# Kernel optimization log

Measured on AMD Instinct MI355X. Metric: run time of the kernel, lower is better.

Reference implementation:

```python
import jax, jax.numpy as jnp
import numpy as np

NUM_NODE = 64   # number of FPS nodes
NSAMPLE = 64    # ball-query / knn group size
RADIUS = 0.3    # first ball-query radius
K_INTERP = 3    # knn for upsample interpolation
BN_EPS = 1e-5


def sqdist(a, b):
    # a [B,S,3], b [B,N,3] -> squared distances [B,S,N]
    return (jnp.sum(a * a, -1)[:, :, None] + jnp.sum(b * b, -1)[:, None, :]
            - 2.0 * jnp.einsum('bsc,bnc->bsn', a, b))


def index_points(points, idx):
    # points [B,C,N] or [B,C,N,1]; idx [B,...] -> gathered [B,C,...]
    if points.ndim == 4:
        points = points[..., 0]
    return jax.vmap(lambda p, i: p[:, i])(points, idx)


def farthest_point_sample(xyz, npoint):
    # xyz [B,3,N] -> idx [B,npoint]; deterministic start at index 0
    B, C, N = xyz.shape

    def body(carry, _):
        dist, far = carry
        centroid = jnp.take_along_axis(xyz, far[:, None, None], axis=2)  # [B,3,1]
        d = jnp.sum((xyz - centroid) ** 2, axis=1)                       # [B,N]
        dist = jnp.minimum(dist, d)
        nxt = jnp.argmax(dist, axis=-1)
        return (dist, nxt), far

    init = (jnp.full((B, N), 1e10, xyz.dtype), jnp.zeros((B,), jnp.int32))
    _, idxs = jax.lax.scan(body, init, None, length=npoint)
    return idxs.T  # [B,npoint]


def query_ball_point(radius, nsample, xyz, new_xyz):
    # xyz [B,3,N], new_xyz [B,3,S] -> group idx [B,S,nsample]
    N = xyz.shape[2]
    sqr = sqdist(jnp.transpose(new_xyz, (0, 2, 1)), jnp.transpose(xyz, (0, 2, 1)))  # [B,S,N]
    if radius is not None:
        idx = jnp.broadcast_to(jnp.arange(N, dtype=jnp.int32), sqr.shape)
        idx = jnp.where(sqr > radius * radius, N, idx)
        idx = jnp.sort(idx, axis=-1)[:, :, :nsample]
        first = idx[:, :, :1]
        idx = jnp.where(idx == N, first, idx)  # pad misses with first hit
    else:
        idx = jnp.argsort(sqr, axis=-1)[:, :, :nsample].astype(jnp.int32)  # knn
    return idx


def _forward(input_fea, input_loc, pred_w, res_w, res_b, bn_gamma, bn_beta):
    # input_fea [B,C,N,1], input_loc [B,3,N]
    fidx = farthest_point_sample(input_loc, NUM_NODE)        # [B,S]
    fpoint_loc = index_points(input_loc, fidx)               # [B,3,S]
    fpoint_fea = index_points(input_fea, fidx)               # [B,C,S]

    gidx = query_ball_point(RADIUS, NSAMPLE, input_loc, fpoint_loc)  # [B,S,K]
    group_fea = index_points(input_fea, gidx) - fpoint_fea[..., None]  # [B,C,S,K]

    # pred_offset: 1x1 conv (no bias) + tanh
    seman = jnp.tanh(jnp.einsum('oc,bcsk->bosk', pred_w, group_fea))  # [B,3,S,K]

    group_loc = index_points(input_loc, gidx) - fpoint_loc[..., None]  # [B,3,S,K]
    node_offset = jnp.mean(seman * group_loc, axis=-1)       # [B,3,S]
    node_loc = fpoint_loc + node_offset                      # [B,3,S]

    gidx2 = query_ball_point(None, NSAMPLE, input_loc, node_loc)  # knn, [B,S,K]

    # residual branch: 1x1 conv + BatchNorm (training-mode batch stats) + ReLU
    res = jnp.einsum('oc,bcnk->bonk', res_w, input_fea) + res_b[None, :, None, None]
    mean = jnp.mean(res, axis=(0, 2, 3), keepdims=True)
    var = jnp.var(res, axis=(0, 2, 3), keepdims=True)
    res = (res - mean) * jax.lax.rsqrt(var + BN_EPS)
    res = jax.nn.relu(res * bn_gamma[None, :, None, None] + bn_beta[None, :, None, None])

    group_res = index_points(res, gidx2)                     # [B,F,S,K]
    node_fea = jnp.max(group_res, axis=-1, keepdims=True)    # [B,F,S,1]

    # upsample_inter: inverse-distance weighted 3-NN interpolation back to N points
    d = sqdist(jnp.transpose(input_loc, (0, 2, 1)), jnp.transpose(node_loc, (0, 2, 1)))  # [B,N,S]
    neg_d, kidx = jax.lax.top_k(-d, K_INTERP)                # k smallest dists
    dists = jnp.maximum(-neg_d, 1e-10)                       # [B,N,k]
    w = 1.0 / dists
    w = w / jnp.sum(w, axis=-1, keepdims=True)               # [B,N,k]
    interp = jnp.sum(index_points(node_fea, kidx) * w[:, None], axis=-1)  # [B,F,N]

    output_fea = jnp.concatenate([input_fea[..., 0], interp], axis=1)[..., None]  # [B,C+F,N,1]
    return output_fea, node_fea, node_offset


def setup_inputs() -> dict:
    key = jax.random.key(0)
    k1, k2, k3, k4, k5 = jax.random.split(key, 5)
    B, C, N = 32, 64, 8192
    FC = 64
    input_fea = jax.random.normal(k1, (B, C, N, 1), dtype=jnp.float32)
    input_loc = jax.random.uniform(k2, (B, 3, N), dtype=jnp.float32)
    pred_w = jax.random.normal(k3, (3, C), dtype=jnp.float32) * (1.0 / np.sqrt(C))
    res_w = jax.random.normal(k4, (FC, C), dtype=jnp.float32) * (1.0 / np.sqrt(C))
    res_b = jnp.zeros((FC,), dtype=jnp.float32)
    bn_gamma = jnp.ones((FC,), dtype=jnp.float32)
    bn_beta = jnp.zeros((FC,), dtype=jnp.float32)
    return {"input_fea": input_fea, "input_loc": input_loc, "pred_w": pred_w,
            "res_w": res_w, "res_b": res_b, "bn_gamma": bn_gamma, "bn_beta": bn_beta}


def reference(input_fea, input_loc, pred_w, res_w, res_b, bn_gamma, bn_beta):
    return _forward(input_fea, input_loc, pred_w, res_w, res_b, bn_gamma, bn_beta)
```

## Files before the change

### kernel.cpp

```cpp
#include <hip/hip_runtime.h>
#include <math.h>

#define BB 32
#define NN 8192
#define CC 64
#define SS 64
#define KK 64

#define WS_FIDX   0
#define WS_FLOC   2048
#define WS_FFEA   8192
#define WS_GIDX   139264
#define WS_NLOC   270336
#define WS_GIDX2  276480
#define WS_PART   407552
#define WS_TOT    2537472
#define WS_SCALE  2541632
#define WS_SHIFT  2541696

__global__ __launch_bounds__(256) void transpose_kernel(const float* __restrict__ fea,
                                                        float* __restrict__ feaT) {
  __shared__ float tile[64 * 65];
  int b = blockIdx.y;
  int n0 = blockIdx.x * 64;
  int t = threadIdx.x;
  const float* fb = fea + (size_t)b * (CC * NN);
#pragma unroll
  for (int m = 0; m < 16; m++) {
    int idx = m * 256 + t;
    int c = idx >> 6, nl = idx & 63;
    tile[c * 65 + nl] = fb[(size_t)c * NN + n0 + nl];
  }
  __syncthreads();
  float* ob = feaT + ((size_t)b * NN + n0) * 64;
#pragma unroll
  for (int m = 0; m < 16; m++) {
    int idx = m * 256 + t;
    int nl = idx >> 6, c = idx & 63;
    ob[idx] = tile[c * 65 + nl];
  }
}

__global__ __launch_bounds__(512, 1) void fps_kernel(const float* __restrict__ loc,
                                                     int* __restrict__ fidx) {
#pragma clang fp contract(off)
  int b = blockIdx.x, t = threadIdx.x;
  const float* lb = loc + (size_t)b * 3 * NN;
  __shared__ float sx[NN], sy[NN], sz[NN];
  __shared__ float wrv[2][8];
  __shared__ int wri[2][8];
  float px[16], py[16], pz[16], dist[16];
#pragma unroll
  for (int k = 0; k < 16; k++) {
    int p = t + 512 * k;
    float x = lb[p], y = lb[NN + p], z = lb[2 * NN + p];
    px[k] = x; py[k] = y; pz[k] = z;
    sx[p] = x; sy[p] = y; sz[p] = z;
    dist[k] = 1e10f;
  }
  __syncthreads();
  int lane = t & 63, w = t >> 6;
  int far = 0;
  for (int it = 0; it < 64; it++) {
    if (t == 0) fidx[b * 64 + it] = far;
    float cx = sx[far], cy = sy[far], cz = sz[far];
    float bv = -1.0f; int bi = 0;
#pragma unroll
    for (int k = 0; k < 16; k++) {
      float dx = px[k] - cx, dy = py[k] - cy, dz = pz[k] - cz;
      float d = (dx * dx + dy * dy) + dz * dz;
      float dm = dist[k];
      dm = d < dm ? d : dm;
      dist[k] = dm;
      if (dm > bv) { bv = dm; bi = t + 512 * k; }
    }
    float v = bv; int vi = bi;
#pragma unroll
    for (int off = 1; off < 64; off <<= 1) {
      float v2 = __shfl_xor(v, off, 64);
      int   i2 = __shfl_xor(vi, off, 64);
      if (v2 > v || (v2 == v && i2 < vi)) { v = v2; vi = i2; }
    }
    int par = it & 1;
    if (lane == 0) { wrv[par][w] = v; wri[par][w] = vi; }
    __syncthreads();
    float gv = wrv[par][0]; int gi = wri[par][0];
#pragma unroll
    for (int w2 = 1; w2 < 8; w2++) {
      float v2 = wrv[par][w2]; int i2 = wri[par][w2];
      if (v2 > gv || (v2 == gv && i2 < gi)) { gv = v2; gi = i2; }
    }
    far = gi;
  }
}

__global__ __launch_bounds__(64) void gather_kernel(const float* __restrict__ loc,
                                                    const float* __restrict__ fea,
                                                    const int* __restrict__ fidx,
                                                    float* __restrict__ floc,
                                                    float* __restrict__ ffea) {
  int bs = blockIdx.x, b = bs >> 6, c = threadIdx.x;
  int g = fidx[bs];
  ffea[bs * 64 + c] = fea[(size_t)b * (CC * NN) + (size_t)c * NN + g];
  if (c < 3) floc[bs * 3 + c] = loc[(size_t)b * (3 * NN) + (size_t)c * NN + g];
}

__global__ __launch_bounds__(256) void ball1_kernel(const float* __restrict__ loc,
                                                    const float* __restrict__ floc,
                                                    int* __restrict__ gidx) {
#pragma clang fp contract(off)
  int w = threadIdx.x >> 6, lane = threadIdx.x & 63;
  int bs = blockIdx.x * 4 + w, b = bs >> 6;
  const float* lb = loc + (size_t)b * 3 * NN;
  float ax = floc[bs * 3], ay = floc[bs * 3 + 1], az = floc[bs * 3 + 2];
  float A = (ax * ax + ay * ay) + az * az;
  int count = 0, firsth = -1;
  for (int ch = 0; ch < 128 && count < 64; ch++) {
    int p = ch * 64 + lane;
    float bx = lb[p], by = lb[NN + p], bz = lb[2 * NN + p];
    float Bn = (bx * bx + by * by) + bz * bz;
    float dot = fmaf(az, bz, fmaf(ay, by, ax * bx));
    float sqr = (A + Bn) - 2.0f * dot;
    bool hit = !(sqr > 0.09f);
    unsigned long long m = __ballot(hit);
    if (m) {
      if (firsth < 0) firsth = ch * 64 + (int)__ffsll(m) - 1;
      int pos = count + (int)__popcll(m & ((1ull << lane) - 1ull));
      if (hit && pos < 64) gidx[bs * 64 + pos] = p;
      count += (int)__popcll(m);
    }
  }
  if (count < 64 && lane >= count) gidx[bs * 64 + lane] = firsth;
}

__global__ __launch_bounds__(64) void seman_kernel(const float* __restrict__ feaT,
                                                   const float* __restrict__ loc,
                                                   const float* __restrict__ pw,
                                                   const int* __restrict__ gidx,
                                                   const float* __restrict__ ffea,
                                                   const float* __restrict__ floc,
                                                   float* __restrict__ out_noff,
                                                   float* __restrict__ nloc) {
  int bs = blockIdx.x, b = bs >> 6, s = bs & 63, k = threadIdx.x;
  __shared__ float sf[64];
  __shared__ float spw[192];
  __shared__ float sl[3];
  sf[k] = ffea[bs * 64 + k];
  spw[k] = pw[k]; spw[64 + k] = pw[64 + k]; spw[128 + k] = pw[128 + k];
  if (k < 3) sl[k] = floc[bs * 3 + k];
  __syncthreads();
  int g = gidx[bs * 64 + k];
  const float* fT = feaT + ((size_t)b * NN + g) * 64;
  float a0 = 0.f, a1 = 0.f, a2 = 0.f;
#pragma unroll
  for (int c4 = 0; c4 < 16; c4++) {
    float4 f = *(const float4*)(fT + 4 * c4);
    int c = 4 * c4;
    float g0 = f.x - sf[c + 0];
    a0 = fmaf(spw[c + 0], g0, a0); a1 = fmaf(spw[64 + c + 0], g0, a1); a2 = fmaf(spw[128 + c + 0], g0, a2);
    float g1 = f.y - sf[c + 1];
    a0 = fmaf(spw[c + 1], g1, a0); a1 = fmaf(spw[64 + c + 1], g1, a1); a2 = fmaf(spw[128 + c + 1], g1, a2);
    float g2 = f.z - sf[c + 2];
    a0 = fmaf(spw[c + 2], g2, a0); a1 = fmaf(spw[64 + c + 2], g2, a1); a2 = fmaf(spw[128 + c + 2], g2, a2);
    float g3 = f.w - sf[c + 3];
    a0 = fmaf(spw[c + 3], g3, a0); a1 = fmaf(spw[64 + c + 3], g3, a1); a2 = fmaf(spw[128 + c + 3], g3, a2);
  }
  const float* lb = loc + (size_t)b * 3 * NN;
  float c0 = tanhf(a0) * (lb[g] - sl[0]);
  float c1 = tanhf(a1) * (lb[NN + g] - sl[1]);
  float c2 = tanhf(a2) * (lb[2 * NN + g] - sl[2]);
#pragma unroll
  for (int off = 32; off; off >>= 1) {
    c0 += __shfl_xor(c0, off, 64);
    c1 += __shfl_xor(c1, off, 64);
    c2 += __shfl_xor(c2, off, 64);
  }
  if (k == 0) {
    float m0 = c0 * (1.0f / 64), m1 = c1 * (1.0f / 64), m2 = c2 * (1.0f / 64);
    out_noff[b * 192 + s] = m0;
    out_noff[b * 192 + 64 + s] = m1;
    out_noff[b * 192 + 128 + s] = m2;
    nloc[bs * 3 + 0] = sl[0] + m0;
    nloc[bs * 3 + 1] = sl[1] + m1;
    nloc[bs * 3 + 2] = sl[2] + m2;
  }
}

__global__ __launch_bounds__(256) void knn_kernel(const float* __restrict__ loc,
                                                  const float* __restrict__ nloc,
                                                  int* __restrict__ gidx2) {
#pragma clang fp contract(off)
  int bs = blockIdx.x, b = bs >> 6, t = threadIdx.x;
  const float* lb = loc + (size_t)b * 3 * NN;
  float ax = nloc[bs * 3], ay = nloc[bs * 3 + 1], az = nloc[bs * 3 + 2];
  float A = (ax * ax + ay * ay) + az * az;
  __shared__ unsigned keys[NN];
  __shared__ unsigned hist[4096];
  __shared__ unsigned part[256];
  __shared__ int sP, sC0, nOut, nCand;
  for (int m = 0; m < 16; m++) hist[m * 256 + t] = 0u;
  if (t == 0) { nOut = 0; nCand = 0; }
  __syncthreads();
  unsigned mykey[32];
#pragma unroll
  for (int k = 0; k < 32; k++) {
    int p = t + 256 * k;
    float bx = lb[p], by = lb[NN + p], bz = lb[2 * NN + p];
    float Bn = (bx * bx + by * by) + bz * bz;
    float dot = fmaf(az, bz, fmaf(ay, by, ax * bx));
    float d = (A + Bn) - 2.0f * dot;
    unsigned kb = __float_as_uint(d);
    kb = (kb & 0x80000000u) ? ~kb : (kb | 0x80000000u);
    mykey[k] = kb;
    keys[p] = kb;
    atomicAdd(&hist[kb >> 20], 1u);
  }
  __syncthreads();
  unsigned ps = 0;
#pragma unroll
  for (int m = 0; m < 16; m++) ps += hist[t * 16 + m];
  part[t] = ps;
  __syncthreads();
  if (t == 0) {
    int cum = 0, seg = 0;
    for (int t2 = 0; t2 < 256; t2++) {
      if (cum + (int)part[t2] >= 64) { seg = t2; break; }
      cum += (int)part[t2];
    }
    int P = seg * 16;
    for (;; P++) {
      if (cum + (int)hist[P] >= 64) break;
      cum += (int)hist[P];
    }
    sP = P; sC0 = cum;
  }
  __syncthreads();
  int P = sP, C0 = sC0;
  unsigned short* cand = (unsigned short*)hist;
  __syncthreads();
#pragma unroll
  for (int k = 0; k < 32; k++) {
    int bin = (int)(mykey[k] >> 20);
    if (bin < P) {
      int pos = atomicAdd(&nOut, 1);
      gidx2[bs * 64 + pos] = t + 256 * k;
    } else if (bin == P) {
      int c = atomicAdd(&nCand, 1);
      cand[c] = (unsigned short)(t + 256 * k);
    }
  }
  __syncthreads();
  if (t < 64) {
    int lane = t;
    int R = 64 - C0, nC = nCand;
    for (int r = 0; r < R; r++) {
      unsigned bk = 0xFFFFFFFFu; int bp = 0x7FFFFFFF, bj = -1;
      for (int j = lane; j < nC; j += 64) {
        int p = cand[j];
        if (p != 0xFFFF) {
          unsigned k2 = keys[p];
          if (k2 < bk || (k2 == bk && p < bp)) { bk = k2; bp = p; bj = j; }
        }
      }
#pragma unroll
      for (int off = 1; off < 64; off <<= 1) {
        unsigned k2 = __shfl_xor(bk, off, 64);
        int p2 = __shfl_xor(bp, off, 64);
        int j2 = __shfl_xor(bj, off, 64);
        if (k2 < bk || (k2 == bk && p2 < bp)) { bk = k2; bp = p2; bj = j2; }
      }
      if (lane == 0) {
        gidx2[bs * 64 + C0 + r] = bp;
        cand[bj] = 0xFFFF;
      }
      __threadfence_block();
    }
  }
}

__global__ __launch_bounds__(256) void cov_kernel(const float* __restrict__ fea,
                                                  float* __restrict__ part) {
  __shared__ float Sf[64 * 133];
  __shared__ float red[4160];
  int t = threadIdx.x, w = t >> 6, lane = t & 63;
  int i = lane >> 3, j = lane & 7;
  float acc[8][8];
  float rs[8];
#pragma unroll
  for (int r = 0; r < 8; r++) {
    rs[r] = 0.f;
#pragma unroll
    for (int r2 = 0; r2 < 8; r2++) acc[r][r2] = 0.f;
  }
  for (int q = 0; q < 4; q++) {
    int chunk = blockIdx.x * 4 + q;
    int p0 = chunk * 128;
    int b = p0 >> 13, n0 = p0 & 8191;
    __syncthreads();
    const float* fb = fea + (size_t)b * (CC * NN) + n0;
    for (int m = 0; m < 32; m++) {
      int idx = m * 256 + t;
      int c = idx >> 7, pt = idx & 127;
      Sf[c * 133 + pt] = fb[(size_t)c * NN + pt];
    }
    __syncthreads();
    for (int pt = w * 32; pt < w * 32 + 32; pt++) {
      float a[8], bv[8];
#pragma unroll
      for (int r = 0; r < 8; r++) {
        a[r] = Sf[(8 * i + r) * 133 + pt];
        bv[r] = Sf[(8 * j + r) * 133 + pt];
      }
#pragma unroll
      for (int r = 0; r < 8; r++) {
        rs[r] += a[r];
#pragma unroll
        for (int r2 = 0; r2 < 8; r2++) acc[r][r2] = fmaf(a[r], bv[r2], acc[r][r2]);
      }
    }
  }
  for (int ww = 0; ww < 4; ww++) {
    if (w == ww) {
#pragma unroll
      for (int r = 0; r < 8; r++) {
#pragma unroll
        for (int r2 = 0; r2 < 8; r2++) {
          int idx = (8 * i + r) * 64 + 8 * j + r2;
          if (ww == 0) red[idx] = acc[r][r2]; else red[idx] += acc[r][r2];
        }
        if (j == 0) {
          int ridx = 4096 + 8 * i + r;
          if (ww == 0) red[ridx] = rs[r]; else red[ridx] += rs[r];
        }
      }
    }
    __syncthreads();
  }
  float* pb = part + (size_t)blockIdx.x * 4160;
  for (int idx = t; idx < 4160; idx += 256) pb[idx] = red[idx];
}

__global__ __launch_bounds__(256) void covreduce_kernel(const float* __restrict__ part,
                                                        float* __restrict__ tot) {
  int e = blockIdx.x * 256 + threadIdx.x;
  if (e >= 4160) return;
  float s = 0.f;
  for (int b2 = 0; b2 < 512; b2++) s += part[(size_t)b2 * 4160 + e];
  tot[e] = s;
}

__global__ __launch_bounds__(64) void bnstats_kernel(const float* __restrict__ tot,
                                                     const float* __restrict__ rw,
                                                     const float* __restrict__ rb,
                                                     const float* __restrict__ gam,
                                                     const float* __restrict__ bet,
                                                     float* __restrict__ bnsc,
                                                     float* __restrict__ bnsh) {
  int o = threadIdx.x;
  const float invM = 1.0f / 262144.0f;
  float mu = 0.f;
  for (int c = 0; c < 64; c++) mu += rw[o * 64 + c] * (tot[4096 + c] * invM);
  float exx = 0.f;
  for (int c = 0; c < 64; c++) {
    const float* row = tot + c * 64;
    float p = 0.f;
    for (int c2 = 0; c2 < 64; c2++) p += rw[o * 64 + c2] * row[c2];
    exx += rw[o * 64 + c] * p;
  }
  exx *= invM;
  float var = exx - mu * mu;
  float mean = mu + rb[o];
  float sc = gam[o] / sqrtf(var + 1e-5f);
  bnsc[o] = sc;
  bnsh[o] = bet[o] - mean * sc;
}

__global__ __launch_bounds__(256) void nodefea_kernel(const float* __restrict__ feaT,
                                                      const float* __restrict__ rw,
                                                      const int* __restrict__ gidx2,
                                                      const float* __restrict__ bnsc,
                                                      const float* __restrict__ bnsh,
                                                      float* __restrict__ out_nf) {
  __shared__ __align__(16) float Lf[4096];
  __shared__ float Lw[4096];
  __shared__ int Lg[64];
  __shared__ float red[256];
  int bs = blockIdx.x, b = bs >> 6, s = bs & 63, t = threadIdx.x;
  if (t < 64) Lg[t] = gidx2[bs * 64 + t];
  __syncthreads();
#pragma unroll
  for (int m = 0; m < 4; m++) {
    int idx4 = m * 256 + t;
    int k = idx4 >> 4, c4 = idx4 & 15;
    float4 f = *(const float4*)(feaT + ((size_t)b * NN + Lg[k]) * 64 + 4 * c4);
    *(float4*)&Lf[idx4 * 4] = f;
  }
  for (int m = 0; m < 16; m++) {
    int idx = m * 256 + t;
    Lw[idx] = rw[(idx & 63) * 64 + (idx >> 6)];
  }
  __syncthreads();
  int o = t & 63, wq = t >> 6;
  float wreg[64];
#pragma unroll
  for (int c = 0; c < 64; c++) wreg[c] = Lw[c * 64 + o];
  float sc = bnsc[o], sh = bnsh[o];
  float mx = -1e30f;
  for (int k = wq * 16; k < wq * 16 + 16; k++) {
    float raw = 0.f;
#pragma unroll
    for (int c4 = 0; c4 < 16; c4++) {
      float4 lf = *(const float4*)&Lf[k * 64 + c4 * 4];
      raw = fmaf(wreg[4 * c4 + 0], lf.x, raw);
      raw = fmaf(wreg[4 * c4 + 1], lf.y, raw);
      raw = fmaf(wreg[4 * c4 + 2], lf.z, raw);
      raw = fmaf(wreg[4 * c4 + 3], lf.w, raw);
    }
    float v = raw * sc + sh;
    v = v > 0.f ? v : 0.f;
    mx = v > mx ? v : mx;
  }
  red[wq * 64 + o] = mx;
  __syncthreads();
  if (t < 64) {
    float m0 = red[t], m1 = red[64 + t], m2 = red[128 + t], m3 = red[192 + t];
    float ma = m0 > m1 ? m0 : m1;
    float mb = m2 > m3 ? m2 : m3;
    float m = ma > mb ? ma : mb;
    out_nf[b * 4096 + t * 64 + s] = m;
  }
}

__global__ __launch_bounds__(256) void interp_kernel(const float* __restrict__ fea,
                                                     const float* __restrict__ loc,
                                                     const float* __restrict__ nloc,
                                                     const float* __restrict__ nf,
                                                     float* __restrict__ out) {
#pragma clang fp contract(off)
  int b = blockIdx.y;
  int t = threadIdx.x;
  int n = blockIdx.x * 256 + t;
  __shared__ float snl[192];
  __shared__ float sB[64];
  if (t < 192) snl[t] = nloc[b * 192 + t];
  __syncthreads();
  if (t < 64) {
    float x = snl[t * 3], y = snl[t * 3 + 1], z = snl[t * 3 + 2];
    sB[t] = (x * x + y * y) + z * z;
  }
  __syncthreads();
  const float* lb = loc + (size_t)b * 3 * NN;
  float px = lb[n], py = lb[NN + n], pz = lb[2 * NN + n];
  float A = (px * px + py * py) + pz * pz;
  float d0 = 1e30f, d1 = 1e30f, d2 = 1e30f;
  int i0 = 0, i1 = 0, i2 = 0;
  for (int s = 0; s < 64; s++) {
    float dot = fmaf(pz, snl[s * 3 + 2], fmaf(py, snl[s * 3 + 1], px * snl[s * 3]));
    float d = (A + sB[s]) - 2.0f * dot;
    if (d < d0) { d2 = d1; i2 = i1; d1 = d0; i1 = i0; d0 = d; i0 = s; }
    else if (d < d1) { d2 = d1; i2 = i1; d1 = d; i1 = s; }
    else if (d < d2) { d2 = d; i2 = s; }
  }
  d0 = d0 > 1e-10f ? d0 : 1e-10f;
  d1 = d1 > 1e-10f ? d1 : 1e-10f;
  d2 = d2 > 1e-10f ? d2 : 1e-10f;
  float r0 = 1.0f / d0, r1 = 1.0f / d1, r2 = 1.0f / d2;
  float rsum = (r0 + r1) + r2;
  float w0 = r0 / rsum, w1 = r1 / rsum, w2 = r2 / rsum;
  const float* nfb = nf + b * 4096;
  const float* fb = fea + (size_t)b * (CC * NN);
  float* ob = out + (size_t)b * (128 * NN);
  for (int o = 0; o < 64; o++) {
    ob[(size_t)o * NN + n] = fb[(size_t)o * NN + n];
    float ip = (nfb[o * 64 + i0] * w0 + nfb[o * 64 + i1] * w1) + nfb[o * 64 + i2] * w2;
    ob[(size_t)(64 + o) * NN + n] = ip;
  }
}

extern "C" void kernel_launch(void* const* d_in, const int* in_sizes, int n_in,
                              void* d_out, int out_size, void* d_ws, size_t ws_size,
                              hipStream_t stream) {
  (void)in_sizes; (void)n_in; (void)out_size; (void)ws_size;
  const float* fea = (const float*)d_in[0];
  const float* loc = (const float*)d_in[1];
  const float* pw  = (const float*)d_in[2];
  const float* rw  = (const float*)d_in[3];
  const float* rb  = (const float*)d_in[4];
  const float* gam = (const float*)d_in[5];
  const float* bet = (const float*)d_in[6];
  float* out = (float*)d_out;
  float* ws = (float*)d_ws;

  int*   fidx  = (int*)(ws + WS_FIDX);
  float* floc  = ws + WS_FLOC;
  float* ffea  = ws + WS_FFEA;
  int*   gidx  = (int*)(ws + WS_GIDX);
  float* nlocp = ws + WS_NLOC;
  int*   gidx2 = (int*)(ws + WS_GIDX2);
  float* part  = ws + WS_PART;
  float* tot   = ws + WS_TOT;
  float* bnsc  = ws + WS_SCALE;
  float* bnsh  = ws + WS_SHIFT;

  float* feaT     = out;
  float* out_nf   = out + 33554432;
  float* out_noff = out + 33685504;

  transpose_kernel<<<dim3(128, 32), dim3(256), 0, stream>>>(fea, feaT);
  fps_kernel<<<dim3(32), dim3(512), 0, stream>>>(loc, fidx);
  gather_kernel<<<dim3(2048), dim3(64), 0, stream>>>(loc, fea, fidx, floc, ffea);
  ball1_kernel<<<dim3(512), dim3(256), 0, stream>>>(loc, floc, gidx);
  seman_kernel<<<dim3(2048), dim3(64), 0, stream>>>(feaT, loc, pw, gidx, ffea, floc, out_noff, nlocp);
  knn_kernel<<<dim3(2048), dim3(256), 0, stream>>>(loc, nlocp, gidx2);
  cov_kernel<<<dim3(512), dim3(256), 0, stream>>>(fea, part);
  covreduce_kernel<<<dim3(17), dim3(256), 0, stream>>>(part, tot);
  bnstats_kernel<<<dim3(1), dim3(64), 0, stream>>>(tot, rw, rb, gam, bet, bnsc, bnsh);
  nodefea_kernel<<<dim3(2048), dim3(256), 0, stream>>>(feaT, rw, gidx2, bnsc, bnsh, out_nf);
  interp_kernel<<<dim3(32, 32), dim3(256), 0, stream>>>(fea, loc, nlocp, out_nf, out);
}
```

Before: 663.6 us.

## Merge independent stages into phase kernels so FPS overlaps transpose and covariance

```diff
diff --git a/kernel.cpp b/kernel.cpp
--- a/kernel.cpp
+++ b/kernel.cpp
@@ -18,61 +18,37 @@
 #define WS_SCALE  2541632
 #define WS_SHIFT  2541696
 
-__global__ __launch_bounds__(256) void transpose_kernel(const float* __restrict__ fea,
-                                                        float* __restrict__ feaT) {
-  __shared__ float tile[64 * 65];
-  int b = blockIdx.y;
-  int n0 = blockIdx.x * 64;
+
+__device__ __forceinline__ void fps_body(int b, const float* __restrict__ loc,
+                                         int* __restrict__ fidx,
+                                         float (*wrv)[4], int (*wri)[4]) {
+#pragma clang fp contract(off)
   int t = threadIdx.x;
-  const float* fb = fea + (size_t)b * (CC * NN);
-#pragma unroll
-  for (int m = 0; m < 16; m++) {
-    int idx = m * 256 + t;
-    int c = idx >> 6, nl = idx & 63;
-    tile[c * 65 + nl] = fb[(size_t)c * NN + n0 + nl];
-  }
-  __syncthreads();
-  float* ob = feaT + ((size_t)b * NN + n0) * 64;
-#pragma unroll
-  for (int m = 0; m < 16; m++) {
-    int idx = m * 256 + t;
-    int nl = idx >> 6, c = idx & 63;
-    ob[idx] = tile[c * 65 + nl];
-  }
-}
-
-__global__ __launch_bounds__(512, 1) void fps_kernel(const float* __restrict__ loc,
-                                                     int* __restrict__ fidx) {
-#pragma clang fp contract(off)
-  int b = blockIdx.x, t = threadIdx.x;
   const float* lb = loc + (size_t)b * 3 * NN;
-  __shared__ float sx[NN], sy[NN], sz[NN];
-  __shared__ float wrv[2][8];
-  __shared__ int wri[2][8];
-  float px[16], py[16], pz[16], dist[16];
-#pragma unroll
-  for (int k = 0; k < 16; k++) {
-    int p = t + 512 * k;
-    float x = lb[p], y = lb[NN + p], z = lb[2 * NN + p];
-    px[k] = x; py[k] = y; pz[k] = z;
-    sx[p] = x; sy[p] = y; sz[p] = z;
+  float px[32], py[32], pz[32], dist[32];
+#pragma unroll
+  for (int k = 0; k < 32; k++) {
+    int p = t + 256 * k;
+    px[k] = lb[p];
+    py[k] = lb[NN + p];
+    pz[k] = lb[2 * NN + p];
     dist[k] = 1e10f;
   }
-  __syncthreads();
   int lane = t & 63, w = t >> 6;
   int far = 0;
   for (int it = 0; it < 64; it++) {
     if (t == 0) fidx[b * 64 + it] = far;
-    float cx = sx[far], cy = sy[far], cz = sz[far];
+    int fs = __builtin_amdgcn_readfirstlane(far);
+    float cx = lb[fs], cy = lb[NN + fs], cz = lb[2 * NN + fs];
     float bv = -1.0f; int bi = 0;
 #pragma unroll
-    for (int k = 0; k < 16; k++) {
+    for (int k = 0; k < 32; k++) {
       float dx = px[k] - cx, dy = py[k] - cy, dz = pz[k] - cz;
       float d = (dx * dx + dy * dy) + dz * dz;
       float dm = dist[k];
       dm = d < dm ? d : dm;
       dist[k] = dm;
-      if (dm > bv) { bv = dm; bi = t + 512 * k; }
+      if (dm > bv) { bv = dm; bi = t + 256 * k; }
     }
     float v = bv; int vi = bi;
 #pragma unroll
@@ -86,7 +62,7 @@
     __syncthreads();
     float gv = wrv[par][0]; int gi = wri[par][0];
 #pragma unroll
-    for (int w2 = 1; w2 < 8; w2++) {
+    for (int w2 = 1; w2 < 4; w2++) {
       float v2 = wrv[par][w2]; int i2 = wri[par][w2];
       if (v2 > gv || (v2 == gv && i2 < gi)) { gv = v2; gi = i2; }
     }
@@ -94,43 +70,186 @@
   }
 }
 
-__global__ __launch_bounds__(64) void gather_kernel(const float* __restrict__ loc,
-                                                    const float* __restrict__ fea,
-                                                    const int* __restrict__ fidx,
-                                                    float* __restrict__ floc,
-                                                    float* __restrict__ ffea) {
-  int bs = blockIdx.x, b = bs >> 6, c = threadIdx.x;
-  int g = fidx[bs];
-  ffea[bs * 64 + c] = fea[(size_t)b * (CC * NN) + (size_t)c * NN + g];
-  if (c < 3) floc[bs * 3 + c] = loc[(size_t)b * (3 * NN) + (size_t)c * NN + g];
-}
-
-__global__ __launch_bounds__(256) void ball1_kernel(const float* __restrict__ loc,
-                                                    const float* __restrict__ floc,
-                                                    int* __restrict__ gidx) {
+__device__ __forceinline__ void transpose_body(int tb, const float* __restrict__ fea,
+                                               float* __restrict__ feaT, float* tile) {
+  int b = tb >> 7;
+  int n0 = (tb & 127) * 64;
+  int t = threadIdx.x;
+  const float* fb = fea + (size_t)b * (CC * NN);
+#pragma unroll
+  for (int m = 0; m < 16; m++) {
+    int idx = m * 256 + t;
+    int c = idx >> 6, nl = idx & 63;
+    tile[c * 65 + nl] = fb[(size_t)c * NN + n0 + nl];
+  }
+  __syncthreads();
+  float* ob = feaT + ((size_t)b * NN + n0) * 64;
+#pragma unroll
+  for (int m = 0; m < 16; m++) {
+    int idx = m * 256 + t;
+    int nl = idx >> 6, c = idx & 63;
+    ob[idx] = tile[c * 65 + nl];
+  }
+}
+
+__device__ __forceinline__ void cov_body(int cb, const float* __restrict__ fea,
+                                         float* __restrict__ part,
+                                         float* Sf, float* red) {
+  int t = threadIdx.x, w = t >> 6, lane = t & 63;
+  int i = lane >> 3, j = lane & 7;
+  float acc[8][8];
+  float rs[8];
+#pragma unroll
+  for (int r = 0; r < 8; r++) {
+    rs[r] = 0.f;
+#pragma unroll
+    for (int r2 = 0; r2 < 8; r2++) acc[r][r2] = 0.f;
+  }
+  for (int q = 0; q < 4; q++) {
+    int chunk = cb * 4 + q;
+    int p0 = chunk * 128;
+    int b = p0 >> 13, n0 = p0 & 8191;
+    __syncthreads();
+    const float* fb = fea + (size_t)b * (CC * NN) + n0;
+    for (int m = 0; m < 32; m++) {
+      int idx = m * 256 + t;
+      int c = idx >> 7, pt = idx & 127;
+      Sf[c * 133 + pt] = fb[(size_t)c * NN + pt];
+    }
+    __syncthreads();
+    for (int pt = w * 32; pt < w * 32 + 32; pt++) {
+      float a[8], bv[8];
+#pragma unroll
+      for (int r = 0; r < 8; r++) {
+        a[r] = Sf[(8 * i + r) * 133 + pt];
+        bv[r] = Sf[(8 * j + r) * 133 + pt];
+      }
+#pragma unroll
+      for (int r = 0; r < 8; r++) {
+        rs[r] += a[r];
+#pragma unroll
+        for (int r2 = 0; r2 < 8; r2++) acc[r][r2] = fmaf(a[r], bv[r2], acc[r][r2]);
+      }
+    }
+  }
+  for (int ww = 0; ww < 4; ww++) {
+    if (w == ww) {
+#pragma unroll
+      for (int r = 0; r < 8; r++) {
+#pragma unroll
+        for (int r2 = 0; r2 < 8; r2++) {
+          int idx = (8 * i + r) * 64 + 8 * j + r2;
+          if (ww == 0) red[idx] = acc[r][r2]; else red[idx] += acc[r][r2];
+        }
+        if (j == 0) {
+          int ridx = 4096 + 8 * i + r;
+          if (ww == 0) red[ridx] = rs[r]; else red[ridx] += rs[r];
+        }
+      }
+    }
+    __syncthreads();
+  }
+  float* pb = part + (size_t)cb * 4160;
+  for (int idx = t; idx < 4160; idx += 256) pb[idx] = red[idx];
+}
+
+__global__ __launch_bounds__(256, 2) void phase1_kernel(const float* __restrict__ fea,
+                                                        const float* __restrict__ loc,
+                                                        float* __restrict__ feaT,
+                                                        int* __restrict__ fidx,
+                                                        float* __restrict__ part) {
+  __shared__ __align__(16) char smem[50688];
+  __shared__ float wrv[2][4];
+  __shared__ int wri[2][4];
+  int blk = blockIdx.x;
+  if (blk < 32) {
+    fps_body(blk, loc, fidx, wrv, wri);
+  } else if (blk < 4128) {
+    transpose_body(blk - 32, fea, feaT, (float*)smem);
+  } else {
+    cov_body(blk - 4128, fea, part, (float*)smem, (float*)(smem + 34048));
+  }
+}
+
+__global__ __launch_bounds__(256) void phase2_kernel(const float* __restrict__ part,
+                                                     float* __restrict__ tot,
+                                                     const float* __restrict__ loc,
+                                                     const float* __restrict__ fea,
+                                                     const int* __restrict__ fidx,
+                                                     float* __restrict__ floc,
+                                                     float* __restrict__ ffea) {
+  int blk = blockIdx.x, t = threadIdx.x;
+  if (blk < 17) {
+    int e = blk * 256 + t;
+    if (e >= 4160) return;
+    float s = 0.f;
+    for (int b2 = 0; b2 < 512; b2++) s += part[(size_t)b2 * 4160 + e];
+    tot[e] = s;
+  } else {
+    int bs = (blk - 17) * 4 + (t >> 6);
+    int c = t & 63;
+    int b = bs >> 6;
+    int g = fidx[bs];
+    ffea[bs * 64 + c] = fea[(size_t)b * (CC * NN) + (size_t)c * NN + g];
+    if (c < 3) floc[bs * 3 + c] = loc[(size_t)b * (3 * NN) + (size_t)c * NN + g];
+  }
+}
+
+__global__ __launch_bounds__(256) void phase3_kernel(const float* __restrict__ loc,
+                                                     const float* __restrict__ floc,
+                                                     int* __restrict__ gidx,
+                                                     const float* __restrict__ tot,
+                                                     const float* __restrict__ rw,
+                                                     const float* __restrict__ rb,
+                                                     const float* __restrict__ gam,
+                                                     const float* __restrict__ bet,
+                                                     float* __restrict__ bnsc,
+                                                     float* __restrict__ bnsh) {
 #pragma clang fp contract(off)
-  int w = threadIdx.x >> 6, lane = threadIdx.x & 63;
-  int bs = blockIdx.x * 4 + w, b = bs >> 6;
-  const float* lb = loc + (size_t)b * 3 * NN;
-  float ax = floc[bs * 3], ay = floc[bs * 3 + 1], az = floc[bs * 3 + 2];
-  float A = (ax * ax + ay * ay) + az * az;
-  int count = 0, firsth = -1;
-  for (int ch = 0; ch < 128 && count < 64; ch++) {
-    int p = ch * 64 + lane;
-    float bx = lb[p], by = lb[NN + p], bz = lb[2 * NN + p];
-    float Bn = (bx * bx + by * by) + bz * bz;
-    float dot = fmaf(az, bz, fmaf(ay, by, ax * bx));
-    float sqr = (A + Bn) - 2.0f * dot;
-    bool hit = !(sqr > 0.09f);
-    unsigned long long m = __ballot(hit);
-    if (m) {
-      if (firsth < 0) firsth = ch * 64 + (int)__ffsll(m) - 1;
-      int pos = count + (int)__popcll(m & ((1ull << lane) - 1ull));
-      if (hit && pos < 64) gidx[bs * 64 + pos] = p;
-      count += (int)__popcll(m);
-    }
-  }
-  if (count < 64 && lane >= count) gidx[bs * 64 + lane] = firsth;
+  int blk = blockIdx.x;
+  if (blk < 512) {
+    int w = threadIdx.x >> 6, lane = threadIdx.x & 63;
+    int bs = blk * 4 + w, b = bs >> 6;
+    const float* lb = loc + (size_t)b * 3 * NN;
+    float ax = floc[bs * 3], ay = floc[bs * 3 + 1], az = floc[bs * 3 + 2];
+    float A = (ax * ax + ay * ay) + az * az;
+    int count = 0, firsth = -1;
+    for (int ch = 0; ch < 128 && count < 64; ch++) {
+      int p = ch * 64 + lane;
+      float bx = lb[p], by = lb[NN + p], bz = lb[2 * NN + p];
+      float Bn = (bx * bx + by * by) + bz * bz;
+      float dot = fmaf(az, bz, fmaf(ay, by, ax * bx));
+      float sqr = (A + Bn) - 2.0f * dot;
+      bool hit = !(sqr > 0.09f);
+      unsigned long long m = __ballot(hit);
+      if (m) {
+        if (firsth < 0) firsth = ch * 64 + (int)__ffsll(m) - 1;
+        int pos = count + (int)__popcll(m & ((1ull << lane) - 1ull));
+        if (hit && pos < 64) gidx[bs * 64 + pos] = p;
+        count += (int)__popcll(m);
+      }
+    }
+    if (count < 64 && lane >= count) gidx[bs * 64 + lane] = firsth;
+  } else {
+    int o = threadIdx.x;
+    if (o >= 64) return;
+    const float invM = 1.0f / 262144.0f;
+    float mu = 0.f;
+    for (int c = 0; c < 64; c++) mu += rw[o * 64 + c] * (tot[4096 + c] * invM);
+    float exx = 0.f;
+    for (int c = 0; c < 64; c++) {
+      const float* row = tot + c * 64;
+      float p = 0.f;
+      for (int c2 = 0; c2 < 64; c2++) p += rw[o * 64 + c2] * row[c2];
+      exx += rw[o * 64 + c] * p;
+    }
+    exx *= invM;
+    float var = exx - mu * mu;
+    float mean = mu + rb[o];
+    float sc = gam[o] / sqrtf(var + 1e-5f);
+    bnsc[o] = sc;
+    bnsh[o] = bet[o] - mean * sc;
+  }
 }
 
 __global__ __launch_bounds__(64) void seman_kernel(const float* __restrict__ feaT,
@@ -278,103 +397,6 @@
   }
 }
 
-__global__ __launch_bounds__(256) void cov_kernel(const float* __restrict__ fea,
-                                                  float* __restrict__ part) {
-  __shared__ float Sf[64 * 133];
-  __shared__ float red[4160];
-  int t = threadIdx.x, w = t >> 6, lane = t & 63;
-  int i = lane >> 3, j = lane & 7;
-  float acc[8][8];
-  float rs[8];
-#pragma unroll
-  for (int r = 0; r < 8; r++) {
-    rs[r] = 0.f;
-#pragma unroll
-    for (int r2 = 0; r2 < 8; r2++) acc[r][r2] = 0.f;
-  }
-  for (int q = 0; q < 4; q++) {
-    int chunk = blockIdx.x * 4 + q;
-    int p0 = chunk * 128;
-    int b = p0 >> 13, n0 = p0 & 8191;
-    __syncthreads();
-    const float* fb = fea + (size_t)b * (CC * NN) + n0;
-    for (int m = 0; m < 32; m++) {
-      int idx = m * 256 + t;
-      int c = idx >> 7, pt = idx & 127;
-      Sf[c * 133 + pt] = fb[(size_t)c * NN + pt];
-    }
-    __syncthreads();
-    for (int pt = w * 32; pt < w * 32 + 32; pt++) {
-      float a[8], bv[8];
-#pragma unroll
-      for (int r = 0; r < 8; r++) {
-        a[r] = Sf[(8 * i + r) * 133 + pt];
-        bv[r] = Sf[(8 * j + r) * 133 + pt];
-      }
-#pragma unroll
-      for (int r = 0; r < 8; r++) {
-        rs[r] += a[r];
-#pragma unroll
-        for (int r2 = 0; r2 < 8; r2++) acc[r][r2] = fmaf(a[r], bv[r2], acc[r][r2]);
-      }
-    }
-  }
-  for (int ww = 0; ww < 4; ww++) {
-    if (w == ww) {
-#pragma unroll
-      for (int r = 0; r < 8; r++) {
-#pragma unroll
-        for (int r2 = 0; r2 < 8; r2++) {
-          int idx = (8 * i + r) * 64 + 8 * j + r2;
-          if (ww == 0) red[idx] = acc[r][r2]; else red[idx] += acc[r][r2];
-        }
-        if (j == 0) {
-          int ridx = 4096 + 8 * i + r;
-          if (ww == 0) red[ridx] = rs[r]; else red[ridx] += rs[r];
-        }
-      }
-    }
-    __syncthreads();
-  }
-  float* pb = part + (size_t)blockIdx.x * 4160;
-  for (int idx = t; idx < 4160; idx += 256) pb[idx] = red[idx];
-}
-
-__global__ __launch_bounds__(256) void covreduce_kernel(const float* __restrict__ part,
-                                                        float* __restrict__ tot) {
-  int e = blockIdx.x * 256 + threadIdx.x;
-  if (e >= 4160) return;
-  float s = 0.f;
-  for (int b2 = 0; b2 < 512; b2++) s += part[(size_t)b2 * 4160 + e];
-  tot[e] = s;
-}
-
-__global__ __launch_bounds__(64) void bnstats_kernel(const float* __restrict__ tot,
-                                                     const float* __restrict__ rw,
-                                                     const float* __restrict__ rb,
-                                                     const float* __restrict__ gam,
-                                                     const float* __restrict__ bet,
-                                                     float* __restrict__ bnsc,
-                                                     float* __restrict__ bnsh) {
-  int o = threadIdx.x;
-  const float invM = 1.0f / 262144.0f;
-  float mu = 0.f;
-  for (int c = 0; c < 64; c++) mu += rw[o * 64 + c] * (tot[4096 + c] * invM);
-  float exx = 0.f;
-  for (int c = 0; c < 64; c++) {
-    const float* row = tot + c * 64;
-    float p = 0.f;
-    for (int c2 = 0; c2 < 64; c2++) p += rw[o * 64 + c2] * row[c2];
-    exx += rw[o * 64 + c] * p;
-  }
-  exx *= invM;
-  float var = exx - mu * mu;
-  float mean = mu + rb[o];
-  float sc = gam[o] / sqrtf(var + 1e-5f);
-  bnsc[o] = sc;
-  bnsh[o] = bet[o] - mean * sc;
-}
-
 __global__ __launch_bounds__(256) void nodefea_kernel(const float* __restrict__ feaT,
                                                       const float* __restrict__ rw,
                                                       const int* __restrict__ gidx2,
@@ -506,15 +528,11 @@
   float* out_nf   = out + 33554432;
   float* out_noff = out + 33685504;
 
-  transpose_kernel<<<dim3(128, 32), dim3(256), 0, stream>>>(fea, feaT);
-  fps_kernel<<<dim3(32), dim3(512), 0, stream>>>(loc, fidx);
-  gather_kernel<<<dim3(2048), dim3(64), 0, stream>>>(loc, fea, fidx, floc, ffea);
-  ball1_kernel<<<dim3(512), dim3(256), 0, stream>>>(loc, floc, gidx);
+  phase1_kernel<<<dim3(4640), dim3(256), 0, stream>>>(fea, loc, feaT, fidx, part);
+  phase2_kernel<<<dim3(529), dim3(256), 0, stream>>>(part, tot, loc, fea, fidx, floc, ffea);
+  phase3_kernel<<<dim3(513), dim3(256), 0, stream>>>(loc, floc, gidx, tot, rw, rb, gam, bet, bnsc, bnsh);
   seman_kernel<<<dim3(2048), dim3(64), 0, stream>>>(feaT, loc, pw, gidx, ffea, floc, out_noff, nlocp);
   knn_kernel<<<dim3(2048), dim3(256), 0, stream>>>(loc, nlocp, gidx2);
-  cov_kernel<<<dim3(512), dim3(256), 0, stream>>>(fea, part);
-  covreduce_kernel<<<dim3(17), dim3(256), 0, stream>>>(part, tot);
-  bnstats_kernel<<<dim3(1), dim3(64), 0, stream>>>(tot, rw, rb, gam, bet, bnsc, bnsh);
   nodefea_kernel<<<dim3(2048), dim3(256), 0, stream>>>(feaT, rw, gidx2, bnsc, bnsh, out_nf);
   interp_kernel<<<dim3(32, 32), dim3(256), 0, stream>>>(fea, loc, nlocp, out_nf, out);
 }
```

New measurement: 564.1 us. -15.0%, faster.
